# Performance work log

Hardware: AMD Instinct MI355X
Metric: run time of the kernel (lower is better)

The kernel has to match this reference:

```python
import jax, jax.numpy as jnp
import numpy as np

N_SAMPLE, N_RES = 1024, 4096

def setup_inputs() -> dict:
    key = jax.random.key(0)
    k1, k2 = jax.random.split(key)
    pred = jax.random.normal(k1, (N_SAMPLE, N_RES, 3), dtype=jnp.float32)
    true = jax.random.normal(k2, (N_RES, 3), dtype=jnp.float32)
    mask = jnp.ones((N_RES,), dtype=jnp.bool_)
    return {"pred_coordinate": pred, "true_coordinate": true, "coordinate_mask": mask}


def _tm_score(pred_coordinate, true_coordinate, coordinate_mask):
    # mask used as weights: identical to torch's boolean gather + reduce
    w = coordinate_mask.astype(jnp.float32)           # [L]
    Lt = jnp.sum(w)                                   # number of valid residues
    # d0 normalization (RNA uses protein formula), clamped at 0.5
    d0 = jnp.where(Lt <= 15.0, 0.5, 1.24 * jnp.cbrt(Lt - 15.0) - 1.8)
    d0 = jnp.maximum(d0, 0.5)
    d0_sq = d0 * d0

    wn = w / Lt                                       # normalized weights [L]
    true_mean = jnp.einsum('l,li->i', wn, true_coordinate)              # [3]
    pred_mean = jnp.einsum('l,sli->si', wn, pred_coordinate)            # [S,3]
    pred_c = pred_coordinate - pred_mean[:, None, :]                    # [S,L,3]
    true_c = true_coordinate - true_mean                                # [L,3]

    # Kabsch: covariance H_s = pred_c^T diag(w) true_c  -> [S,3,3]
    H = jnp.einsum('sli,l,lj->sij', pred_c, w, true_c)
    U, _, Vt = jnp.linalg.svd(H, full_matrices=False)
    V = jnp.swapaxes(Vt, -1, -2)
    # proper rotation (no reflection): flip sign of last singular vector if det<0
    det = jnp.linalg.det(jnp.einsum('sij,skj->sik', V, U))              # det(V U^T)
    D = jnp.stack([jnp.ones_like(det), jnp.ones_like(det), jnp.sign(det)], axis=-1)  # [S,3]
    R = jnp.einsum('sij,sj,skj->sik', V, D, U)        # R = V diag(D) U^T, [S,3,3]

    aligned = jnp.einsum('sij,slj->sli', R, pred_c) + true_mean         # [S,L,3]
    d_sq = jnp.sum((aligned - true_coordinate) ** 2, axis=-1)           # [S,L]
    terms = 1.0 / (1.0 + d_sq / d0_sq)
    tm = jnp.einsum('sl,l->s', terms, wn)             # masked mean -> [S]
    return tm


def reference(pred_coordinate, true_coordinate, coordinate_mask):
    return _tm_score(pred_coordinate, true_coordinate, coordinate_mask)
```

## Files before the change

### kernel.cpp

```cpp
#include <hip/hip_runtime.h>
#include <math.h>


#define NS   1024
#define NL   4096
#define TPB  256
#define CHUNKS 4

#define WSA_OFF 0
#define WSB_OFF 16384

__device__ __forceinline__ float waveReduceSum(float v) {
    #pragma unroll
    for (int off = 32; off > 0; off >>= 1)
        v += __shfl_down(v, off, 64);
    return v;
}

__global__ __launch_bounds__(TPB) void k1_cov(
    const float* __restrict__ pred, const float* __restrict__ tru,
    const int* __restrict__ mask, float* __restrict__ ws)
{
    const int s   = blockIdx.x;
    const int tid = threadIdx.x;
    const int wave = tid >> 6, lane = tid & 63;
    const float* ps = pred + (size_t)s * NL * 3;

    float acc[16];
    #pragma unroll
    for (int i = 0; i < 16; ++i) acc[i] = 0.f;

    #pragma unroll
    for (int k = 0; k < CHUNKS; ++k) {
        const int rbase = k * (NL / CHUNKS) + tid * 4;
        const float4* pp = (const float4*)(ps + (size_t)rbase * 3);
        const float4* tp = (const float4*)(tru + (size_t)rbase * 3);
        const int4    mi = *(const int4*)(mask + rbase);
        const float4 q0 = pp[0], q1 = pp[1], q2 = pp[2];
        const float4 u0 = tp[0], u1 = tp[1], u2 = tp[2];

        const float px[4] = {q0.x, q0.w, q1.z, q2.y};
        const float py[4] = {q0.y, q1.x, q1.w, q2.z};
        const float pz[4] = {q0.z, q1.y, q2.x, q2.w};
        const float tx[4] = {u0.x, u0.w, u1.z, u2.y};
        const float ty[4] = {u0.y, u1.x, u1.w, u2.z};
        const float tz[4] = {u0.z, u1.y, u2.x, u2.w};
        const float wm[4] = {mi.x ? 1.f : 0.f, mi.y ? 1.f : 0.f,
                             mi.z ? 1.f : 0.f, mi.w ? 1.f : 0.f};

        #pragma unroll
        for (int r = 0; r < 4; ++r) {
            const float w = wm[r];
            const float wpx = w * px[r], wpy = w * py[r], wpz = w * pz[r];
            acc[0] += w;
            acc[1] += w * tx[r]; acc[2] += w * ty[r]; acc[3] += w * tz[r];
            acc[4] += wpx; acc[5] += wpy; acc[6] += wpz;
            acc[7]  += wpx * tx[r]; acc[8]  += wpx * ty[r]; acc[9]  += wpx * tz[r];
            acc[10] += wpy * tx[r]; acc[11] += wpy * ty[r]; acc[12] += wpy * tz[r];
            acc[13] += wpz * tx[r]; acc[14] += wpz * ty[r]; acc[15] += wpz * tz[r];
        }
    }

    __shared__ float sred[4][16];
    #pragma unroll
    for (int i = 0; i < 16; ++i) {
        float r = waveReduceSum(acc[i]);
        if (lane == 0) sred[wave][i] = r;
    }
    __syncthreads();
    if (tid < 16) {
        ws[WSA_OFF + (size_t)s * 16 + tid] =
            sred[0][tid] + sred[1][tid] + sred[2][tid] + sred[3][tid];
    }
}

__global__ __launch_bounds__(TPB) void k2_kabsch(float* __restrict__ ws)
{
    const int sid = blockIdx.x * TPB + threadIdx.x;
    if (sid >= NS) return;

    const float* base = ws + WSA_OFF + (size_t)sid * 16;
    double S[16];
    #pragma unroll
    for (int i = 0; i < 16; ++i) S[i] = (double)base[i];

    const double Lt = S[0], invLt = 1.0 / Lt;
    const double tmx = S[1]*invLt, tmy = S[2]*invLt, tmz = S[3]*invLt;
    const double pmx = S[4]*invLt, pmy = S[5]*invLt, pmz = S[6]*invLt;

    float H[3][3];
    const double Sp[3] = {S[4], S[5], S[6]};
    const double St[3] = {S[1], S[2], S[3]};
    #pragma unroll
    for (int i = 0; i < 3; ++i)
        #pragma unroll
        for (int j = 0; j < 3; ++j)
            H[i][j] = (float)((S[7 + i*3 + j] - Sp[i]*St[j]*invLt) * invLt);

    const float Sxx=H[0][0], Sxy=H[0][1], Sxz=H[0][2];
    const float Syx=H[1][0], Syy=H[1][1], Syz=H[1][2];
    const float Szx=H[2][0], Szy=H[2][1], Szz=H[2][2];
    float A[4][4] = {
      { Sxx+Syy+Szz, Syz-Szy,      Szx-Sxz,      Sxy-Syx      },
      { Syz-Szy,     Sxx-Syy-Szz,  Sxy+Syx,      Szx+Sxz      },
      { Szx-Sxz,     Sxy+Syx,      Syy-Sxx-Szz,  Syz+Szy      },
      { Sxy-Syx,     Szx+Sxz,      Syz+Szy,      Szz-Sxx-Syy  }
    };
    float V[4][4] = {{1,0,0,0},{0,1,0,0},{0,0,1,0},{0,0,0,1}};

    for (int sweep = 0; sweep < 8; ++sweep) {
        for (int p = 0; p < 3; ++p) for (int q = p+1; q < 4; ++q) {
            const float apq = A[p][q];
            if (fabsf(apq) < 1e-30f) continue;
            const float tau = (A[q][q] - A[p][p]) / (2.0f * apq);
            const float tt  = (tau >= 0.0f ? 1.0f : -1.0f)
                              / (fabsf(tau) + sqrtf(1.0f + tau*tau));
            const float cc  = 1.0f / sqrtf(1.0f + tt*tt);
            const float sn  = tt * cc;
            #pragma unroll
            for (int k = 0; k < 4; ++k) {
                const float akp = A[k][p], akq = A[k][q];
                A[k][p] = cc*akp - sn*akq;
                A[k][q] = sn*akp + cc*akq;
            }
            #pragma unroll
            for (int k = 0; k < 4; ++k) {
                const float apk = A[p][k], aqk = A[q][k];
                A[p][k] = cc*apk - sn*aqk;
                A[q][k] = sn*apk + cc*aqk;
            }
            #pragma unroll
            for (int k = 0; k < 4; ++k) {
                const float vkp = V[k][p], vkq = V[k][q];
                V[k][p] = cc*vkp - sn*vkq;
                V[k][q] = sn*vkp + cc*vkq;
            }
        }
    }
    int im = 0;
    #pragma unroll
    for (int i = 1; i < 4; ++i) if (A[i][i] > A[im][im]) im = i;
    const float q0 = V[0][im], qx = V[1][im], qy = V[2][im], qz = V[3][im];

    const float R00 = q0*q0+qx*qx-qy*qy-qz*qz;
    const float R01 = 2.0f*(qx*qy - q0*qz);
    const float R02 = 2.0f*(qx*qz + q0*qy);
    const float R10 = 2.0f*(qy*qx + q0*qz);
    const float R11 = q0*q0-qx*qx+qy*qy-qz*qz;
    const float R12 = 2.0f*(qy*qz - q0*qx);
    const float R20 = 2.0f*(qz*qx - q0*qy);
    const float R21 = 2.0f*(qz*qy + q0*qx);
    const float R22 = q0*q0-qx*qx-qy*qy+qz*qz;

    double d0 = (Lt <= 15.0) ? 0.5 : (1.24 * cbrt(Lt - 15.0) - 1.8);
    if (d0 < 0.5) d0 = 0.5;
    const double inv_d0sq = 1.0 / (d0 * d0);

    float* o = ws + WSB_OFF + (size_t)sid * 20;
    o[0]=R00; o[1]=R01; o[2]=R02;
    o[3]=R10; o[4]=R11; o[5]=R12;
    o[6]=R20; o[7]=R21; o[8]=R22;
    o[9]=(float)pmx; o[10]=(float)pmy; o[11]=(float)pmz;
    o[12]=(float)tmx; o[13]=(float)tmy; o[14]=(float)tmz;
    o[15]=(float)inv_d0sq; o[16]=(float)invLt;
    o[17]=0.f; o[18]=0.f; o[19]=0.f;
}

__global__ __launch_bounds__(TPB) void k3_score(
    const float* __restrict__ pred, const float* __restrict__ tru,
    const int* __restrict__ mask, const float* __restrict__ ws,
    float* __restrict__ out)
{
    const int s   = blockIdx.x;
    const int tid = threadIdx.x;
    const int wave = tid >> 6, lane = tid & 63;
    const float* ps = pred + (size_t)s * NL * 3;

    const float4* bp = (const float4*)(ws + WSB_OFF + (size_t)s * 20);
    const float4 b0 = bp[0], b1 = bp[1], b2 = bp[2], b3 = bp[3], b4 = bp[4];
    const float R00=b0.x, R01=b0.y, R02=b0.z, R10=b0.w;
    const float R11=b1.x, R12=b1.y, R20=b1.z, R21=b1.w;
    const float R22=b2.x, pmx=b2.y, pmy=b2.z, pmz=b2.w;
    const float tmx=b3.x, tmy=b3.y, tmz=b3.z, inv_d0sq=b3.w;
    const float invLt=b4.x;

    float tacc = 0.f;
    #pragma unroll
    for (int k = 0; k < CHUNKS; ++k) {
        const int rbase = k * (NL / CHUNKS) + tid * 4;
        const float4* pp = (const float4*)(ps + (size_t)rbase * 3);
        const float4* tp = (const float4*)(tru + (size_t)rbase * 3);
        const int4    mi = *(const int4*)(mask + rbase);
        const float4 q0 = pp[0], q1 = pp[1], q2 = pp[2];
        const float4 u0 = tp[0], u1 = tp[1], u2 = tp[2];

        const float px[4] = {q0.x, q0.w, q1.z, q2.y};
        const float py[4] = {q0.y, q1.x, q1.w, q2.z};
        const float pz[4] = {q0.z, q1.y, q2.x, q2.w};
        const float tx[4] = {u0.x, u0.w, u1.z, u2.y};
        const float ty[4] = {u0.y, u1.x, u1.w, u2.z};
        const float tz[4] = {u0.z, u1.y, u2.x, u2.w};
        const float wm[4] = {mi.x ? 1.f : 0.f, mi.y ? 1.f : 0.f,
                             mi.z ? 1.f : 0.f, mi.w ? 1.f : 0.f};

        #pragma unroll
        for (int r = 0; r < 4; ++r) {
            const float vx = px[r] - pmx, vy = py[r] - pmy, vz = pz[r] - pmz;
            const float a0 = R00*vx + R01*vy + R02*vz + tmx - tx[r];
            const float a1 = R10*vx + R11*vy + R12*vz + tmy - ty[r];
            const float a2 = R20*vx + R21*vy + R22*vz + tmz - tz[r];
            const float dsq = a0*a0 + a1*a1 + a2*a2;
            tacc += wm[r] * __builtin_amdgcn_rcpf(1.0f + dsq * inv_d0sq);
        }
    }
    tacc *= invLt;

    __shared__ float sred[4];
    float r = waveReduceSum(tacc);
    if (lane == 0) sred[wave] = r;
    __syncthreads();
    if (tid == 0)
        out[s] = sred[0] + sred[1] + sred[2] + sred[3];
}

extern "C" void kernel_launch(void* const* d_in, const int* in_sizes, int n_in,
                              void* d_out, int out_size, void* d_ws, size_t ws_size,
                              hipStream_t stream) {
    const float* pred = (const float*)d_in[0];
    const float* tru  = (const float*)d_in[1];
    const int*   mask = (const int*)d_in[2];
    float* out = (float*)d_out;
    float* ws  = (float*)d_ws;

    k1_cov   <<<NS, TPB, 0, stream>>>(pred, tru, mask, ws);
    k2_kabsch<<<(NS + TPB - 1) / TPB, TPB, 0, stream>>>(ws);
    k3_score <<<NS, TPB, 0, stream>>>(pred, tru, mask, ws, out);
}
```

Baseline: 120.9 us.

## Fuse covariance, Kabsch solve and scoring into one per-sample kernel

Merges the three kernels into a single kernel per sample. Each block computes its covariance sums, solves for the optimal quaternion redundantly in every thread using a closed-form quartic (Newton on the characteristic polynomial plus adjugate eigenvector) instead of Jacobi sweeps, then scores. Global loads are now staged through LDS with coalesced float4 copies. The intent is to drop two launches and the workspace round trip. In exchange every thread runs serial double-precision eigen-solving, extra barriers are added per chunk, and each block reads pred twice in a row, so the second read likely hits cache.

```diff
diff --git a/kernel.cpp b/kernel.cpp
--- a/kernel.cpp
+++ b/kernel.cpp
@@ -2,13 +2,11 @@
 #include <math.h>
 
 
-#define NS   1024
-#define NL   4096
-#define TPB  256
-#define CHUNKS 4
-
-#define WSA_OFF 0
-#define WSB_OFF 16384
+#define NS        1024
+#define NL        4096
+#define TPB       256
+#define CHUNK_RES 1024
+#define NCHUNK    4
 
 __device__ __forceinline__ float waveReduceSum(float v) {
     #pragma unroll
@@ -17,27 +15,49 @@
     return v;
 }
 
-__global__ __launch_bounds__(TPB) void k1_cov(
+__device__ __forceinline__ double det3(const double B[4][4],
+                                       int r0, int r1, int r2,
+                                       int c0, int c1, int c2) {
+    return B[r0][c0]*(B[r1][c1]*B[r2][c2] - B[r1][c2]*B[r2][c1])
+         - B[r0][c1]*(B[r1][c0]*B[r2][c2] - B[r1][c2]*B[r2][c0])
+         + B[r0][c2]*(B[r1][c0]*B[r2][c1] - B[r1][c1]*B[r2][c0]);
+}
+
+__global__ __launch_bounds__(TPB, 4) void tm_fused(
     const float* __restrict__ pred, const float* __restrict__ tru,
-    const int* __restrict__ mask, float* __restrict__ ws)
+    const int* __restrict__ mask, float* __restrict__ out)
 {
-    const int s   = blockIdx.x;
-    const int tid = threadIdx.x;
+    const int s    = blockIdx.x;
+    const int tid  = threadIdx.x;
     const int wave = tid >> 6, lane = tid & 63;
     const float* ps = pred + (size_t)s * NL * 3;
 
-    float acc[16];
-    #pragma unroll
-    for (int i = 0; i < 16; ++i) acc[i] = 0.f;
-
-    #pragma unroll
-    for (int k = 0; k < CHUNKS; ++k) {
-        const int rbase = k * (NL / CHUNKS) + tid * 4;
-        const float4* pp = (const float4*)(ps + (size_t)rbase * 3);
-        const float4* tp = (const float4*)(tru + (size_t)rbase * 3);
-        const int4    mi = *(const int4*)(mask + rbase);
-        const float4 q0 = pp[0], q1 = pp[1], q2 = pp[2];
-        const float4 u0 = tp[0], u1 = tp[1], u2 = tp[2];
+    __shared__ float ldsP[CHUNK_RES * 3];
+    __shared__ float ldsT[CHUNK_RES * 3];
+    __shared__ float sred[4][18];
+
+    float acc[18];
+    #pragma unroll
+    for (int i = 0; i < 18; ++i) acc[i] = 0.f;
+
+    for (int k = 0; k < NCHUNK; ++k) {
+        const float4* gp = (const float4*)(ps  + (size_t)k * CHUNK_RES * 3);
+        const float4* gt = (const float4*)(tru + (size_t)k * CHUNK_RES * 3);
+        float4* lp = (float4*)ldsP;
+        float4* lt = (float4*)ldsT;
+        #pragma unroll
+        for (int j = 0; j < 3; ++j) {
+            const int idx = wave * 192 + j * 64 + lane;
+            lp[idx] = gp[idx];
+            lt[idx] = gt[idx];
+        }
+        __syncthreads();
+
+        const float4* rp = (const float4*)&ldsP[tid * 12];
+        const float4* rt = (const float4*)&ldsT[tid * 12];
+        const float4 q0 = rp[0], q1 = rp[1], q2 = rp[2];
+        const float4 u0 = rt[0], u1 = rt[1], u2 = rt[2];
+        const int4   mi = *(const int4*)(mask + k * CHUNK_RES + tid * 4);
 
         const float px[4] = {q0.x, q0.w, q1.z, q2.y};
         const float py[4] = {q0.y, q1.x, q1.w, q2.z};
@@ -58,141 +78,131 @@
             acc[7]  += wpx * tx[r]; acc[8]  += wpx * ty[r]; acc[9]  += wpx * tz[r];
             acc[10] += wpy * tx[r]; acc[11] += wpy * ty[r]; acc[12] += wpy * tz[r];
             acc[13] += wpz * tx[r]; acc[14] += wpz * ty[r]; acc[15] += wpz * tz[r];
-        }
-    }
-
-    __shared__ float sred[4][16];
-    #pragma unroll
-    for (int i = 0; i < 16; ++i) {
+            acc[16] += wpx * px[r] + wpy * py[r] + wpz * pz[r];
+            acc[17] += w * (tx[r]*tx[r] + ty[r]*ty[r] + tz[r]*tz[r]);
+        }
+        __syncthreads();
+    }
+
+    #pragma unroll
+    for (int i = 0; i < 18; ++i) {
         float r = waveReduceSum(acc[i]);
         if (lane == 0) sred[wave][i] = r;
     }
     __syncthreads();
-    if (tid < 16) {
-        ws[WSA_OFF + (size_t)s * 16 + tid] =
-            sred[0][tid] + sred[1][tid] + sred[2][tid] + sred[3][tid];
-    }
-}
-
-__global__ __launch_bounds__(TPB) void k2_kabsch(float* __restrict__ ws)
-{
-    const int sid = blockIdx.x * TPB + threadIdx.x;
-    if (sid >= NS) return;
-
-    const float* base = ws + WSA_OFF + (size_t)sid * 16;
-    double S[16];
-    #pragma unroll
-    for (int i = 0; i < 16; ++i) S[i] = (double)base[i];
+
+    double S[18];
+    #pragma unroll
+    for (int i = 0; i < 18; ++i)
+        S[i] = (double)sred[0][i] + (double)sred[1][i]
+             + (double)sred[2][i] + (double)sred[3][i];
 
     const double Lt = S[0], invLt = 1.0 / Lt;
-    const double tmx = S[1]*invLt, tmy = S[2]*invLt, tmz = S[3]*invLt;
-    const double pmx = S[4]*invLt, pmy = S[5]*invLt, pmz = S[6]*invLt;
-
-    float H[3][3];
+    const double tmxd = S[1]*invLt, tmyd = S[2]*invLt, tmzd = S[3]*invLt;
+    const double pmxd = S[4]*invLt, pmyd = S[5]*invLt, pmzd = S[6]*invLt;
+
+    double HA[3][3];
     const double Sp[3] = {S[4], S[5], S[6]};
     const double St[3] = {S[1], S[2], S[3]};
     #pragma unroll
     for (int i = 0; i < 3; ++i)
         #pragma unroll
         for (int j = 0; j < 3; ++j)
-            H[i][j] = (float)((S[7 + i*3 + j] - Sp[i]*St[j]*invLt) * invLt);
-
-    const float Sxx=H[0][0], Sxy=H[0][1], Sxz=H[0][2];
-    const float Syx=H[1][0], Syy=H[1][1], Syz=H[1][2];
-    const float Szx=H[2][0], Szy=H[2][1], Szz=H[2][2];
-    float A[4][4] = {
+            HA[i][j] = (S[7 + i*3 + j] - Sp[i]*St[j]*invLt) * invLt;
+    const double gA = (S[16] - (Sp[0]*Sp[0]+Sp[1]*Sp[1]+Sp[2]*Sp[2])*invLt) * invLt;
+    const double gB = (S[17] - (St[0]*St[0]+St[1]*St[1]+St[2]*St[2])*invLt) * invLt;
+
+    const double Sxx=HA[0][0], Sxy=HA[0][1], Sxz=HA[0][2];
+    const double Syx=HA[1][0], Syy=HA[1][1], Syz=HA[1][2];
+    const double Szx=HA[2][0], Szy=HA[2][1], Szz=HA[2][2];
+    double K[4][4] = {
       { Sxx+Syy+Szz, Syz-Szy,      Szx-Sxz,      Sxy-Syx      },
       { Syz-Szy,     Sxx-Syy-Szz,  Sxy+Syx,      Szx+Sxz      },
       { Szx-Sxz,     Sxy+Syx,      Syy-Sxx-Szz,  Syz+Szy      },
       { Sxy-Syx,     Szx+Sxz,      Syz+Szy,      Szz-Sxx-Syy  }
     };
-    float V[4][4] = {{1,0,0,0},{0,1,0,0},{0,0,1,0},{0,0,0,1}};
-
-    for (int sweep = 0; sweep < 8; ++sweep) {
-        for (int p = 0; p < 3; ++p) for (int q = p+1; q < 4; ++q) {
-            const float apq = A[p][q];
-            if (fabsf(apq) < 1e-30f) continue;
-            const float tau = (A[q][q] - A[p][p]) / (2.0f * apq);
-            const float tt  = (tau >= 0.0f ? 1.0f : -1.0f)
-                              / (fabsf(tau) + sqrtf(1.0f + tau*tau));
-            const float cc  = 1.0f / sqrtf(1.0f + tt*tt);
-            const float sn  = tt * cc;
+
+    double E2 = 0.0;
+    #pragma unroll
+    for (int i = 0; i < 4; ++i)
+        #pragma unroll
+        for (int j = 0; j < 4; ++j)
+            if (j > i) E2 += K[i][i]*K[j][j] - K[i][j]*K[i][j];
+    const double E3 = det3(K,1,2,3, 1,2,3) + det3(K,0,2,3, 0,2,3)
+                    + det3(K,0,1,3, 0,1,3) + det3(K,0,1,2, 0,1,2);
+    const double E4 = K[0][0]*det3(K,1,2,3, 1,2,3) - K[0][1]*det3(K,1,2,3, 0,2,3)
+                    + K[0][2]*det3(K,1,2,3, 0,1,3) - K[0][3]*det3(K,1,2,3, 0,1,2);
+
+    double lam = 0.5 * (gA + gB);
+    #pragma unroll
+    for (int it = 0; it < 8; ++it) {
+        const double l2 = lam * lam;
+        const double P  = ((l2 + E2) * lam - E3) * lam + E4;
+        const double Pd = (4.0 * l2 + 2.0 * E2) * lam - E3;
+        if (fabs(Pd) < 1e-300) break;
+        lam -= P / Pd;
+    }
+
+    #pragma unroll
+    for (int i = 0; i < 4; ++i) K[i][i] -= lam;
+    double best[4] = {1.0, 0.0, 0.0, 0.0};
+    double bestn = -1.0;
+    #pragma unroll
+    for (int r = 0; r < 4; ++r) {
+        int ri[3]; int t = 0;
+        #pragma unroll
+        for (int i = 0; i < 4; ++i) if (i != r) ri[t++] = i;
+        double v[4];
+        #pragma unroll
+        for (int c = 0; c < 4; ++c) {
+            int cj[3]; t = 0;
             #pragma unroll
-            for (int k = 0; k < 4; ++k) {
-                const float akp = A[k][p], akq = A[k][q];
-                A[k][p] = cc*akp - sn*akq;
-                A[k][q] = sn*akp + cc*akq;
-            }
-            #pragma unroll
-            for (int k = 0; k < 4; ++k) {
-                const float apk = A[p][k], aqk = A[q][k];
-                A[p][k] = cc*apk - sn*aqk;
-                A[q][k] = sn*apk + cc*aqk;
-            }
-            #pragma unroll
-            for (int k = 0; k < 4; ++k) {
-                const float vkp = V[k][p], vkq = V[k][q];
-                V[k][p] = cc*vkp - sn*vkq;
-                V[k][q] = sn*vkp + cc*vkq;
-            }
-        }
-    }
-    int im = 0;
-    #pragma unroll
-    for (int i = 1; i < 4; ++i) if (A[i][i] > A[im][im]) im = i;
-    const float q0 = V[0][im], qx = V[1][im], qy = V[2][im], qz = V[3][im];
-
-    const float R00 = q0*q0+qx*qx-qy*qy-qz*qz;
-    const float R01 = 2.0f*(qx*qy - q0*qz);
-    const float R02 = 2.0f*(qx*qz + q0*qy);
-    const float R10 = 2.0f*(qy*qx + q0*qz);
-    const float R11 = q0*q0-qx*qx+qy*qy-qz*qz;
-    const float R12 = 2.0f*(qy*qz - q0*qx);
-    const float R20 = 2.0f*(qz*qx - q0*qy);
-    const float R21 = 2.0f*(qz*qy + q0*qx);
-    const float R22 = q0*q0-qx*qx-qy*qy+qz*qz;
+            for (int j = 0; j < 4; ++j) if (j != c) cj[t++] = j;
+            const double d = det3(K, ri[0],ri[1],ri[2], cj[0],cj[1],cj[2]);
+            v[c] = ((r + c) & 1) ? -d : d;
+        }
+        const double n = v[0]*v[0]+v[1]*v[1]+v[2]*v[2]+v[3]*v[3];
+        if (n > bestn) { bestn = n; best[0]=v[0]; best[1]=v[1]; best[2]=v[2]; best[3]=v[3]; }
+    }
+    const double qn = 1.0 / sqrt(bestn);
+    const double q0d = best[0]*qn, qxd = best[1]*qn, qyd = best[2]*qn, qzd = best[3]*qn;
+
+    const float R00 = (float)(q0d*q0d+qxd*qxd-qyd*qyd-qzd*qzd);
+    const float R01 = (float)(2.0*(qxd*qyd - q0d*qzd));
+    const float R02 = (float)(2.0*(qxd*qzd + q0d*qyd));
+    const float R10 = (float)(2.0*(qyd*qxd + q0d*qzd));
+    const float R11 = (float)(q0d*q0d-qxd*qxd+qyd*qyd-qzd*qzd);
+    const float R12 = (float)(2.0*(qyd*qzd - q0d*qxd));
+    const float R20 = (float)(2.0*(qzd*qxd - q0d*qyd));
+    const float R21 = (float)(2.0*(qzd*qyd + q0d*qxd));
+    const float R22 = (float)(q0d*q0d-qxd*qxd-qyd*qyd+qzd*qzd);
 
     double d0 = (Lt <= 15.0) ? 0.5 : (1.24 * cbrt(Lt - 15.0) - 1.8);
     if (d0 < 0.5) d0 = 0.5;
-    const double inv_d0sq = 1.0 / (d0 * d0);
-
-    float* o = ws + WSB_OFF + (size_t)sid * 20;
-    o[0]=R00; o[1]=R01; o[2]=R02;
-    o[3]=R10; o[4]=R11; o[5]=R12;
-    o[6]=R20; o[7]=R21; o[8]=R22;
-    o[9]=(float)pmx; o[10]=(float)pmy; o[11]=(float)pmz;
-    o[12]=(float)tmx; o[13]=(float)tmy; o[14]=(float)tmz;
-    o[15]=(float)inv_d0sq; o[16]=(float)invLt;
-    o[17]=0.f; o[18]=0.f; o[19]=0.f;
-}
-
-__global__ __launch_bounds__(TPB) void k3_score(
-    const float* __restrict__ pred, const float* __restrict__ tru,
-    const int* __restrict__ mask, const float* __restrict__ ws,
-    float* __restrict__ out)
-{
-    const int s   = blockIdx.x;
-    const int tid = threadIdx.x;
-    const int wave = tid >> 6, lane = tid & 63;
-    const float* ps = pred + (size_t)s * NL * 3;
-
-    const float4* bp = (const float4*)(ws + WSB_OFF + (size_t)s * 20);
-    const float4 b0 = bp[0], b1 = bp[1], b2 = bp[2], b3 = bp[3], b4 = bp[4];
-    const float R00=b0.x, R01=b0.y, R02=b0.z, R10=b0.w;
-    const float R11=b1.x, R12=b1.y, R20=b1.z, R21=b1.w;
-    const float R22=b2.x, pmx=b2.y, pmy=b2.z, pmz=b2.w;
-    const float tmx=b3.x, tmy=b3.y, tmz=b3.z, inv_d0sq=b3.w;
-    const float invLt=b4.x;
+    const float inv_d0sq = (float)(1.0 / (d0 * d0));
+    const float invLtf   = (float)invLt;
+    const float pmx = (float)pmxd, pmy = (float)pmyd, pmz = (float)pmzd;
+    const float tmx = (float)tmxd, tmy = (float)tmyd, tmz = (float)tmzd;
 
     float tacc = 0.f;
-    #pragma unroll
-    for (int k = 0; k < CHUNKS; ++k) {
-        const int rbase = k * (NL / CHUNKS) + tid * 4;
-        const float4* pp = (const float4*)(ps + (size_t)rbase * 3);
-        const float4* tp = (const float4*)(tru + (size_t)rbase * 3);
-        const int4    mi = *(const int4*)(mask + rbase);
-        const float4 q0 = pp[0], q1 = pp[1], q2 = pp[2];
-        const float4 u0 = tp[0], u1 = tp[1], u2 = tp[2];
+    for (int k = 0; k < NCHUNK; ++k) {
+        const float4* gp = (const float4*)(ps  + (size_t)k * CHUNK_RES * 3);
+        const float4* gt = (const float4*)(tru + (size_t)k * CHUNK_RES * 3);
+        float4* lp = (float4*)ldsP;
+        float4* lt = (float4*)ldsT;
+        #pragma unroll
+        for (int j = 0; j < 3; ++j) {
+            const int idx = wave * 192 + j * 64 + lane;
+            lp[idx] = gp[idx];
+            lt[idx] = gt[idx];
+        }
+        __syncthreads();
+
+        const float4* rp = (const float4*)&ldsP[tid * 12];
+        const float4* rt = (const float4*)&ldsT[tid * 12];
+        const float4 q0 = rp[0], q1 = rp[1], q2 = rp[2];
+        const float4 u0 = rt[0], u1 = rt[1], u2 = rt[2];
+        const int4   mi = *(const int4*)(mask + k * CHUNK_RES + tid * 4);
 
         const float px[4] = {q0.x, q0.w, q1.z, q2.y};
         const float py[4] = {q0.y, q1.x, q1.w, q2.z};
@@ -212,15 +222,15 @@
             const float dsq = a0*a0 + a1*a1 + a2*a2;
             tacc += wm[r] * __builtin_amdgcn_rcpf(1.0f + dsq * inv_d0sq);
         }
-    }
-    tacc *= invLt;
-
-    __shared__ float sred[4];
+        __syncthreads();
+    }
+    tacc *= invLtf;
+
     float r = waveReduceSum(tacc);
-    if (lane == 0) sred[wave] = r;
+    if (lane == 0) sred[wave][0] = r;
     __syncthreads();
     if (tid == 0)
-        out[s] = sred[0] + sred[1] + sred[2] + sred[3];
+        out[s] = sred[0][0] + sred[1][0] + sred[2][0] + sred[3][0];
 }
 
 extern "C" void kernel_launch(void* const* d_in, const int* in_sizes, int n_in,
@@ -230,9 +240,6 @@
     const float* tru  = (const float*)d_in[1];
     const int*   mask = (const int*)d_in[2];
     float* out = (float*)d_out;
-    float* ws  = (float*)d_ws;
-
-    k1_cov   <<<NS, TPB, 0, stream>>>(pred, tru, mask, ws);
-    k2_kabsch<<<(NS + TPB - 1) / TPB, TPB, 0, stream>>>(ws);
-    k3_score <<<NS, TPB, 0, stream>>>(pred, tru, mask, ws, out);
-}
+    (void)d_ws; (void)ws_size;
+    tm_fused<<<NS, TPB, 0, stream>>>(pred, tru, mask, out);
+}
```

After: 99.14 us. -18.0%, faster.
